# Optimization experiments

Measured on AMD Instinct MI355X. Metric: run time of the kernel, lower is better.

Reference implementation:

```python
import jax, jax.numpy as jnp
import numpy as np

DIM = 512
HEADS = 8
DHEAD = 64
INNER = HEADS * DHEAD
CHUNK = 8
GAMMA = 1.0
EPS = 1e-8
LN_EPS = 1e-5


def setup_inputs() -> dict:
    key = jax.random.key(0)
    ks = jax.random.split(key, 10)
    B, N = 64, 256
    return {
        "q": jax.random.normal(ks[0], (B, N, DIM), jnp.float32),
        "k": jax.random.normal(ks[1], (B, N, DIM), jnp.float32),
        "v": jax.random.normal(ks[2], (B, N, DIM), jnp.float32),
        "ln_gamma": jnp.ones((DIM,), jnp.float32),
        "ln_beta": jnp.zeros((DIM,), jnp.float32),
        "W_in": jax.random.normal(ks[3], (DIM, INNER), jnp.float32) / np.sqrt(DIM),
        "W_out": jax.random.normal(ks[4], (INNER, DIM), jnp.float32) / np.sqrt(INNER),
        "b_out": jnp.zeros((DIM,), jnp.float32),
        "cov_logit": jnp.asarray(0.6, jnp.float32),
        "var_logit": jnp.asarray(0.2, jnp.float32),
        "use_advanced": 1,
    }


def _layernorm(x, g, b):
    mu = jnp.mean(x, axis=-1, keepdims=True)
    var = jnp.mean(jnp.square(x - mu), axis=-1, keepdims=True)
    return (x - mu) * jax.lax.rsqrt(var + LN_EPS) * g + b


def _transform(t, ln_gamma, ln_beta, W_in):
    # [B,N,dim] -> [h,B,N,d]
    B, N, _ = t.shape
    f = _layernorm(t, ln_gamma, ln_beta) @ W_in
    return f.reshape(B, N, HEADS, DHEAD).transpose(2, 0, 1, 3)


def _chunk_stats(E):
    # E: [M, N, d], chunks of size CHUNK over M. Returns per-chunk scalars V, C of shape [M//CHUNK].
    M, N, d = E.shape
    nc = M // CHUNK
    Ec = E.reshape(nc, CHUNK, N, d)
    # variance component: torch.var is unbiased (ddof=1) over seq dim
    sigma = jnp.sqrt(jnp.var(Ec, axis=2, ddof=1) + EPS)  # [nc, CHUNK, d]
    V = jnp.mean(jax.nn.relu(GAMMA - sigma), axis=(1, 2))  # [nc]
    # covariance component: per-sample off-diagonal energy, averaged per chunk
    centered = Ec - jnp.mean(Ec, axis=2, keepdims=True)
    cov = jnp.einsum("csni,csnj->csij", centered, centered) / (N - 1)  # [nc,CHUNK,d,d]
    total = jnp.sum(jnp.square(cov), axis=(2, 3))
    diag = jnp.sum(jnp.square(jnp.diagonal(cov, axis1=2, axis2=3)), axis=2)
    C = jnp.mean((total - diag) / d, axis=1)  # [nc]
    return V, C


def reference(q, k, v, ln_gamma, ln_beta, W_in, W_out, b_out, cov_logit, var_logit, use_advanced):
    f_q = _transform(q, ln_gamma, ln_beta, W_in)  # [h,B,N,d]
    f_k = _transform(k, ln_gamma, ln_beta, W_in)
    f_v = _transform(v, ln_gamma, ln_beta, W_in)
    h, B, N, d = f_q.shape

    # cosine similarity
    dots_qk = jnp.einsum("hbnd,hbmd->hbnm", f_q, f_k)
    qn = jnp.linalg.norm(f_q, axis=-1)  # [h,B,N]
    kn = jnp.linalg.norm(f_k, axis=-1)
    cosine_sim = dots_qk / (qn[..., :, None] * kn[..., None, :])

    if use_advanced:
        Vq, Cq = _chunk_stats(f_q.reshape(h * B, N, d))
        Vk, Ck = _chunk_stats(f_k.reshape(h * B, N, d))
        var_component = jnp.repeat(Vq * Vk, CHUNK).reshape(h, B, 1, 1)
        cov_component = jnp.repeat(Cq * Ck, CHUNK).reshape(h, B, 1, 1)
    else:
        qc = f_q - jnp.mean(f_q, axis=-1, keepdims=True)
        kc = f_k - jnp.mean(f_k, axis=-1, keepdims=True)
        cov_component = jnp.einsum("hbnd,hbmd->hbnm", qc, kc) / d
        q_var = jnp.var(f_q, axis=-1, ddof=1, keepdims=True)  # [h,B,N,1]
        k_var = jnp.var(f_k, axis=-1, ddof=1, keepdims=True)
        var_component = (q_var * jnp.swapaxes(k_var, -1, -2)) / d

    cov_w = jax.nn.sigmoid(cov_logit)
    var_w = jax.nn.sigmoid(var_logit)
    cos_w = 1.0 - cov_w - var_w
    dots = cos_w * cosine_sim + cov_w * cov_component + var_w * var_component
    out = jnp.einsum("hbnm,hbmd->hbnd", dots, f_v)
    out = out.transpose(1, 2, 0, 3).reshape(B, N, h * d)
    return out @ W_out + b_out
```

## Files before the change

### kernel.cpp

```cpp
#include <hip/hip_runtime.h>
#include <cstdint>
#include <cstddef>

#define DIM    512
#define HEADS  8
#define DHEAD  64
#define NSEQ   256
#define BATCH  64
#define NROWS  (BATCH * NSEQ)
#define HB     (HEADS * BATCH)

typedef unsigned short u16;
typedef __bf16 bf16x8 __attribute__((ext_vector_type(8)));
typedef float  f32x4  __attribute__((ext_vector_type(4)));

__device__ __forceinline__ float sigmoidf_(float x) { return 1.0f / (1.0f + expf(-x)); }

__device__ __forceinline__ u16 f2bf(float f) {
    union { float f; unsigned u; } a; a.f = f;
    return (u16)((a.u + 0x7fffu + ((a.u >> 16) & 1u)) >> 16);
}

__device__ __forceinline__ void gload16(const void* g, void* l) {
    __builtin_amdgcn_global_load_lds((const __attribute__((address_space(1))) void*)g,
                                     (__attribute__((address_space(3))) void*)l, 16, 0, 0);
}

__global__ __launch_bounds__(256)
void transpose_cast_kernel(const float* __restrict__ W0, const float* __restrict__ W1,
                           u16* __restrict__ WT)
{
    __shared__ float tile[64][65];
    const int t = threadIdx.x;
    const int bx = blockIdx.x * 64, by = blockIdx.y * 64;
    const float* W = blockIdx.z ? W1 : W0;
    u16* dst = WT + (size_t)blockIdx.z * 512 * 512;
#pragma unroll
    for (int i = 0; i < 16; ++i) {
        int idx = i * 256 + t, r = idx >> 6, c = idx & 63;
        tile[r][c] = W[(size_t)(by + r) * DIM + bx + c];
    }
    __syncthreads();
#pragma unroll
    for (int i = 0; i < 16; ++i) {
        int idx = i * 256 + t, r = idx >> 6, c = idx & 63;
        dst[(size_t)(bx + r) * DIM + by + c] = f2bf(tile[c][r]);
    }
}

__global__ __launch_bounds__(256)
void ln_cast_kernel(const float* __restrict__ qp, const float* __restrict__ kp,
                    const float* __restrict__ vp, const float* __restrict__ gam,
                    const float* __restrict__ bet, u16* __restrict__ out)
{
    const int wid = threadIdx.x >> 6, lane = threadIdx.x & 63;
    const int row = blockIdx.x * 4 + wid;
    const int tns = row >> 14, lr = row & 16383;
    const float* X = (tns == 0) ? qp : (tns == 1) ? kp : vp;
    const float* xr = X + (size_t)lr * DIM;
    float4 a = *(const float4*)(xr + lane * 8);
    float4 b = *(const float4*)(xr + lane * 8 + 4);
    float v[8] = {a.x, a.y, a.z, a.w, b.x, b.y, b.z, b.w};
    float s = 0.f;
#pragma unroll
    for (int i = 0; i < 8; ++i) s += v[i];
#pragma unroll
    for (int o = 32; o > 0; o >>= 1) s += __shfl_xor(s, o, 64);
    const float mu = s * (1.f / DIM);
    float sq = 0.f;
#pragma unroll
    for (int i = 0; i < 8; ++i) { float d = v[i] - mu; sq += d * d; }
#pragma unroll
    for (int o = 32; o > 0; o >>= 1) sq += __shfl_xor(sq, o, 64);
    const float rstd = rsqrtf(sq * (1.f / DIM) + 1e-5f);
    float4 g0 = *(const float4*)(gam + lane * 8), g1 = *(const float4*)(gam + lane * 8 + 4);
    float4 b0 = *(const float4*)(bet + lane * 8), b1 = *(const float4*)(bet + lane * 8 + 4);
    float gv[8] = {g0.x, g0.y, g0.z, g0.w, g1.x, g1.y, g1.z, g1.w};
    float bv[8] = {b0.x, b0.y, b0.z, b0.w, b1.x, b1.y, b1.z, b1.w};
    union { u16 h[8]; uint4 u; } o16;
#pragma unroll
    for (int i = 0; i < 8; ++i) o16.h[i] = f2bf((v[i] - mu) * rstd * gv[i] + bv[i]);
    *(uint4*)(out + (size_t)row * DIM + lane * 8) = o16.u;
}

__global__ __launch_bounds__(256)
void in_gemm_kernel(const u16* __restrict__ A, const u16* __restrict__ BT,
                    u16* __restrict__ FT, u16* __restrict__ Fseq)
{
    __shared__ u16 shm[128 * 136];
    u16* As = shm;
    u16* Bs = shm + 4096;
    u16* Ct = shm;
    const int t = threadIdx.x, lane = t & 63, w = t >> 6;
    const int wr = w >> 1, wc = w & 1;
    const int c0 = blockIdx.x * 128, r0 = blockIdx.y * 128;
    const int cl = lane & 15, q = lane >> 4;

    f32x4 acc[4][4];
#pragma unroll
    for (int i = 0; i < 4; ++i)
#pragma unroll
        for (int j = 0; j < 4; ++j) acc[i][j] = (f32x4){0.f, 0.f, 0.f, 0.f};

    for (int k0 = 0; k0 < DIM; k0 += 32) {
#pragma unroll
        for (int i = 0; i < 2; ++i) {
            int idx = i * 256 + t;
            int row = idx >> 2, ch = idx & 3;
            gload16(A  + (size_t)(r0 + row) * DIM + k0 + ch * 8, As + idx * 8);
            gload16(BT + (size_t)(c0 + row) * DIM + k0 + ch * 8, Bs + idx * 8);
        }
        __syncthreads();
        bf16x8 af[4], bfr[4];
#pragma unroll
        for (int mi = 0; mi < 4; ++mi)
            af[mi] = *(const bf16x8*)(As + (wr * 64 + mi * 16 + cl) * 32 + q * 8);
#pragma unroll
        for (int ni = 0; ni < 4; ++ni)
            bfr[ni] = *(const bf16x8*)(Bs + (wc * 64 + ni * 16 + cl) * 32 + q * 8);
#pragma unroll
        for (int mi = 0; mi < 4; ++mi)
#pragma unroll
            for (int ni = 0; ni < 4; ++ni)
                acc[mi][ni] = __builtin_amdgcn_mfma_f32_16x16x32_bf16(af[mi], bfr[ni],
                                                                      acc[mi][ni], 0, 0, 0);
        __syncthreads();
    }

    const int tns = r0 >> 14, b = (r0 >> 8) & 63, n0 = r0 & 255;
    const int lr0 = r0 & 16383;

    if (tns == 0) {
#pragma unroll
        for (int mi = 0; mi < 4; ++mi) {
            int lrow = wr * 64 + mi * 16 + q * 4;
#pragma unroll
            for (int ni = 0; ni < 4; ++ni) {
                int lcol = wc * 64 + ni * 16 + cl;
#pragma unroll
                for (int r = 0; r < 4; ++r)
                    Ct[(lrow + r) * 136 + lcol] = f2bf(acc[mi][ni][r]);
            }
        }
        __syncthreads();
#pragma unroll
        for (int i = 0; i < 8; ++i) {
            int idx = t + 256 * i, row = idx >> 4, ch = idx & 15;
            *(uint4*)(Fseq + (size_t)(lr0 + row) * DIM + c0 + ch * 8) =
                *(const uint4*)(Ct + row * 136 + ch * 8);
        }
        __syncthreads();
    }
#pragma unroll
    for (int mi = 0; mi < 4; ++mi) {
        int lrow = wr * 64 + mi * 16 + q * 4;
#pragma unroll
        for (int ni = 0; ni < 4; ++ni) {
            int lcol = wc * 64 + ni * 16 + cl;
#pragma unroll
            for (int r = 0; r < 4; ++r)
                Ct[lcol * 136 + lrow + r] = f2bf(acc[mi][ni][r]);
        }
    }
    __syncthreads();
#pragma unroll
    for (int i = 0; i < 8; ++i) {
        int idx = t + 256 * i, lc = idx >> 4, ch = idx & 15;
        *(uint4*)(FT + (((size_t)(tns * 64 + b) * 512 + c0 + lc) * 256 + n0 + ch * 8)) =
            *(const uint4*)(Ct + lc * 136 + ch * 8);
    }
}

__global__ __launch_bounds__(256)
void stats_kernel(const u16* __restrict__ FT, float* __restrict__ norms,
                  float2* __restrict__ vc)
{
    __shared__ u16 ET[64 * 264];
    __shared__ float mu[64];
    __shared__ float red[4][64];
    __shared__ float wr3[4][3];
    const int hb = blockIdx.x, tns = blockIdx.y, h = hb >> 6, b = hb & 63;
    const int t = threadIdx.x, lane = t & 63, w = t >> 6, cl = lane & 15, q = lane >> 4;
    const size_t Fb = ((size_t)(tns * 64 + b) * 512 + h * 64) * 256;

#pragma unroll
    for (int i = 0; i < 8; ++i) {
        int idx = t + 256 * i;
        int row = idx >> 5, ch = idx & 31;
        *(bf16x8*)(ET + row * 264 + ch * 8) =
            *(const bf16x8*)(FT + Fb + (size_t)row * 256 + ch * 8);
    }
    __syncthreads();

    {
        float s = 0.f;
#pragma unroll
        for (int d = 0; d < 64; ++d) {
            float x = (float)*(const __bf16*)(ET + d * 264 + t);
            s += x * x;
        }
        norms[((size_t)tns * HB + hb) * 256 + t] = sqrtf(s);
    }
    {
        int d = t & 63, part = t >> 6;
        float s = 0.f;
#pragma unroll
        for (int i = 0; i < 8; ++i) {
            bf16x8 v8 = *(const bf16x8*)(ET + d * 264 + part * 64 + i * 8);
#pragma unroll
            for (int j = 0; j < 8; ++j) s += (float)v8[j];
        }
        red[part][d] = s;
    }
    __syncthreads();
    if (t < 64) mu[t] = (red[0][t] + red[1][t] + red[2][t] + red[3][t]) * (1.f / 256.f);
    __syncthreads();

    f32x4 g[4];
#pragma unroll
    for (int nj = 0; nj < 4; ++nj) g[nj] = (f32x4){0.f, 0.f, 0.f, 0.f};
#pragma unroll
    for (int ks = 0; ks < 8; ++ks) {
        bf16x8 af = *(const bf16x8*)(ET + (16 * w + cl) * 264 + ks * 32 + q * 8);
#pragma unroll
        for (int nj = 0; nj < 4; ++nj) {
            bf16x8 bfr = *(const bf16x8*)(ET + (16 * nj + cl) * 264 + ks * 32 + q * 8);
            g[nj] = __builtin_amdgcn_mfma_f32_16x16x32_bf16(af, bfr, g[nj], 0, 0, 0);
        }
    }
    float t2 = 0.f, d2 = 0.f, vs = 0.f;
#pragma unroll
    for (int nj = 0; nj < 4; ++nj) {
        int j = 16 * nj + cl;
        float mj = mu[j];
#pragma unroll
        for (int r = 0; r < 4; ++r) {
            int i = 16 * w + 4 * q + r;
            float gc = (g[nj][r] - 256.f * mu[i] * mj) * (1.f / 255.f);
            float g2 = gc * gc;
            t2 += g2;
            if (i == j) {
                d2 += g2;
                float sig = sqrtf(gc + 1e-8f);
                vs += fmaxf(1.f - sig, 0.f);
            }
        }
    }
#pragma unroll
    for (int o = 32; o > 0; o >>= 1) {
        t2 += __shfl_xor(t2, o, 64);
        d2 += __shfl_xor(d2, o, 64);
        vs += __shfl_xor(vs, o, 64);
    }
    if (lane == 0) { wr3[w][0] = t2; wr3[w][1] = d2; wr3[w][2] = vs; }
    __syncthreads();
    if (t == 0) {
        float T = 0.f, D = 0.f, V = 0.f;
        for (int i = 0; i < 4; ++i) { T += wr3[i][0]; D += wr3[i][1]; V += wr3[i][2]; }
        vc[(size_t)tns * HB + hb] = make_float2(V * (1.f / 64.f), (T - D) * (1.f / 64.f));
    }
}

__global__ __launch_bounds__(256)
void attn_kernel(const u16* __restrict__ FT, const u16* __restrict__ Fseq,
                 const float* __restrict__ norms, const float2* __restrict__ vc,
                 const float* __restrict__ cov_logit, const float* __restrict__ var_logit,
                 u16* __restrict__ G)
{
    __shared__ u16 pool[256 * 72];
    __shared__ u16 MT[64 * 72];
    __shared__ float invq[256], invk[256], sv[64];
    const int hb = blockIdx.x, h = hb >> 6, b = hb & 63;
    const int t = threadIdx.x, lane = t & 63, w = t >> 6, cl = lane & 15, q = lane >> 4;
    u16* KT = pool;
    u16* VT = pool + 64 * 136;

    const float cw = sigmoidf_(*cov_logit), vw = sigmoidf_(*var_logit);
    const float cosw = 1.f - cw - vw;
    float s_hb;
    {
        int basec = hb & ~7;
        float vq = 0, cq = 0, vk = 0, ck = 0;
#pragma unroll
        for (int m = 0; m < 8; ++m) {
            float2 a = vc[basec + m];       vq += a.x; cq += a.y;
            float2 bb = vc[HB + basec + m]; vk += bb.x; ck += bb.y;
        }
        s_hb = (cw * cq * ck + vw * vq * vk) * (1.f / 64.f);
    }

    invq[t] = 1.f / norms[((size_t)0 * HB + hb) * 256 + t];
    invk[t] = 1.f / norms[((size_t)1 * HB + hb) * 256 + t];
    __syncthreads();

    const size_t FTk = ((size_t)(1 * 64 + b) * 512 + h * 64) * 256;
    const size_t FTv = ((size_t)(2 * 64 + b) * 512 + h * 64) * 256;
    f32x4 acc1[4];
#pragma unroll
    for (int nj = 0; nj < 4; ++nj) acc1[nj] = (f32x4){0.f, 0.f, 0.f, 0.f};
    float sp[4] = {0.f, 0.f, 0.f, 0.f};

    for (int c = 0; c < 2; ++c) {
#pragma unroll
        for (int i = 0; i < 4; ++i) {
            int idx = t + 256 * i;
            int row = idx >> 4, ch = idx & 15;
            int n0 = c * 128 + ch * 8;
            bf16x8 kv = *(const bf16x8*)(FT + FTk + (size_t)row * 256 + n0);
            bf16x8 vv = *(const bf16x8*)(FT + FTv + (size_t)row * 256 + n0);
            bf16x8 ksc;
#pragma unroll
            for (int j = 0; j < 8; ++j) ksc[j] = (__bf16)((float)kv[j] * invk[n0 + j]);
            *(bf16x8*)(KT + row * 136 + ch * 8) = ksc;
            *(bf16x8*)(VT + row * 136 + ch * 8) = vv;
        }
        __syncthreads();
#pragma unroll
        for (int ks = 0; ks < 4; ++ks) {
            bf16x8 af = *(const bf16x8*)(KT + (16 * w + cl) * 136 + ks * 32 + q * 8);
#pragma unroll
            for (int nj = 0; nj < 4; ++nj) {
                bf16x8 bfr = *(const bf16x8*)(VT + (16 * nj + cl) * 136 + ks * 32 + q * 8);
                if (w == 0) {
                    float s = 0.f;
#pragma unroll
                    for (int j = 0; j < 8; ++j) s += (float)bfr[j];
                    sp[nj] += s;
                }
                acc1[nj] = __builtin_amdgcn_mfma_f32_16x16x32_bf16(af, bfr, acc1[nj], 0, 0, 0);
            }
        }
        __syncthreads();
    }
    if (w == 0) {
#pragma unroll
        for (int nj = 0; nj < 4; ++nj) {
            float s = sp[nj];
            s += __shfl_xor(s, 16, 64);
            s += __shfl_xor(s, 32, 64);
            if (q == 0) sv[16 * nj + cl] = s;
        }
    }
#pragma unroll
    for (int nj = 0; nj < 4; ++nj)
#pragma unroll
        for (int r = 0; r < 4; ++r)
            MT[(16 * nj + cl) * 72 + 16 * w + 4 * q + r] = f2bf(acc1[nj][r]);
    __syncthreads();

    f32x4 acc2[4][4];
#pragma unroll
    for (int mi = 0; mi < 4; ++mi)
#pragma unroll
        for (int nj = 0; nj < 4; ++nj) acc2[mi][nj] = (f32x4){0.f, 0.f, 0.f, 0.f};
    const size_t Fq = (size_t)(b * 256) * DIM + h * 64;
#pragma unroll
    for (int ks2 = 0; ks2 < 2; ++ks2) {
        bf16x8 bfm[4];
#pragma unroll
        for (int nj = 0; nj < 4; ++nj)
            bfm[nj] = *(const bf16x8*)(MT + (16 * nj + cl) * 72 + ks2 * 32 + q * 8);
#pragma unroll
        for (int mi = 0; mi < 4; ++mi) {
            bf16x8 aq = *(const bf16x8*)(Fseq + Fq +
                         (size_t)(64 * w + 16 * mi + cl) * DIM + ks2 * 32 + q * 8);
#pragma unroll
            for (int nj = 0; nj < 4; ++nj)
                acc2[mi][nj] = __builtin_amdgcn_mfma_f32_16x16x32_bf16(aq, bfm[nj],
                                                                       acc2[mi][nj], 0, 0, 0);
        }
    }
    __syncthreads();
    u16* Os = pool;
#pragma unroll
    for (int mi = 0; mi < 4; ++mi) {
        int nbase = 64 * w + 16 * mi + 4 * q;
#pragma unroll
        for (int nj = 0; nj < 4; ++nj) {
            int j = 16 * nj + cl;
            float svj = sv[j];
#pragma unroll
            for (int r = 0; r < 4; ++r) {
                float o = cosw * acc2[mi][nj][r] * invq[nbase + r] + s_hb * svj;
                Os[(nbase + r) * 72 + j] = f2bf(o);
            }
        }
    }
    __syncthreads();
#pragma unroll
    for (int i = 0; i < 8; ++i) {
        int cidx = t + 256 * i;
        int row = cidx >> 3, ch = cidx & 7;
        *(uint4*)(G + (size_t)(b * 256 + row) * DIM + h * 64 + ch * 8) =
            *(const uint4*)(Os + row * 72 + ch * 8);
    }
}

__global__ __launch_bounds__(256)
void out_gemm_kernel(const u16* __restrict__ A, const u16* __restrict__ BT,
                     const float* __restrict__ bias, float* __restrict__ C)
{
    __shared__ u16 As[128 * 32];
    __shared__ u16 Bs[128 * 32];
    const int t = threadIdx.x, lane = t & 63, w = t >> 6;
    const int wr = w >> 1, wc = w & 1;
    const int c0 = blockIdx.x * 128, r0 = blockIdx.y * 128;
    const int cl = lane & 15, q = lane >> 4;

    f32x4 acc[4][4];
#pragma unroll
    for (int i = 0; i < 4; ++i)
#pragma unroll
        for (int j = 0; j < 4; ++j) acc[i][j] = (f32x4){0.f, 0.f, 0.f, 0.f};

    for (int k0 = 0; k0 < DIM; k0 += 32) {
#pragma unroll
        for (int i = 0; i < 2; ++i) {
            int idx = i * 256 + t;
            int row = idx >> 2, ch = idx & 3;
            gload16(A  + (size_t)(r0 + row) * DIM + k0 + ch * 8, As + idx * 8);
            gload16(BT + (size_t)(c0 + row) * DIM + k0 + ch * 8, Bs + idx * 8);
        }
        __syncthreads();
        bf16x8 af[4], bfr[4];
#pragma unroll
        for (int mi = 0; mi < 4; ++mi)
            af[mi] = *(const bf16x8*)(As + (wr * 64 + mi * 16 + cl) * 32 + q * 8);
#pragma unroll
        for (int ni = 0; ni < 4; ++ni)
            bfr[ni] = *(const bf16x8*)(Bs + (wc * 64 + ni * 16 + cl) * 32 + q * 8);
#pragma unroll
        for (int mi = 0; mi < 4; ++mi)
#pragma unroll
            for (int ni = 0; ni < 4; ++ni)
                acc[mi][ni] = __builtin_amdgcn_mfma_f32_16x16x32_bf16(af[mi], bfr[ni],
                                                                      acc[mi][ni], 0, 0, 0);
        __syncthreads();
    }
#pragma unroll
    for (int mi = 0; mi < 4; ++mi) {
        int row0 = r0 + wr * 64 + mi * 16 + q * 4;
#pragma unroll
        for (int ni = 0; ni < 4; ++ni) {
            int col = c0 + wc * 64 + ni * 16 + cl;
            float bv = bias[col];
#pragma unroll
            for (int r = 0; r < 4; ++r)
                C[(size_t)(row0 + r) * DIM + col] = acc[mi][ni][r] + bv;
        }
    }
}

extern "C" void kernel_launch(void* const* d_in, const int* in_sizes, int n_in,
                              void* d_out, int out_size, void* d_ws, size_t ws_size,
                              hipStream_t stream)
{
    const float* q         = (const float*)d_in[0];
    const float* k         = (const float*)d_in[1];
    const float* v         = (const float*)d_in[2];
    const float* ln_g      = (const float*)d_in[3];
    const float* ln_b      = (const float*)d_in[4];
    const float* W_in      = (const float*)d_in[5];
    const float* W_out     = (const float*)d_in[6];
    const float* b_out     = (const float*)d_in[7];
    const float* cov_logit = (const float*)d_in[8];
    const float* var_logit = (const float*)d_in[9];
    float* out = (float*)d_out;

    char* base = (char*)d_ws;
    u16*    Abf   = (u16*)base;
    u16*    WT    = (u16*)(base + 50331648);
    u16*    FT    = (u16*)(base + 51380224);
    u16*    Fseq  = (u16*)(base + 101711872);
    float*  norms = (float*)(base + 118489088);
    float2* vc    = (float2*)(base + 119537664);
    u16*    Gb    = Abf;

    transpose_cast_kernel<<<dim3(8, 8, 2), 256, 0, stream>>>(W_in, W_out, WT);
    ln_cast_kernel<<<dim3(3 * NROWS / 4), 256, 0, stream>>>(q, k, v, ln_g, ln_b, Abf);
    in_gemm_kernel<<<dim3(4, 3 * NROWS / 128), 256, 0, stream>>>(Abf, WT, FT, Fseq);
    stats_kernel<<<dim3(HB, 2), 256, 0, stream>>>(FT, norms, vc);
    attn_kernel<<<dim3(HB), 256, 0, stream>>>(FT, Fseq, norms, vc,
                                              cov_logit, var_logit, Gb);
    out_gemm_kernel<<<dim3(4, NROWS / 128), 256, 0, stream>>>(
        Gb, WT + 512 * 512, b_out, out);
}
```

Baseline: 245.1 us.

## Fold LayerNorm into input GEMM via weight prescaling and epilogue correction

```diff
diff --git a/kernel.cpp b/kernel.cpp
--- a/kernel.cpp
+++ b/kernel.cpp
@@ -28,13 +28,16 @@
 
 __global__ __launch_bounds__(256)
 void transpose_cast_kernel(const float* __restrict__ W0, const float* __restrict__ W1,
-                           u16* __restrict__ WT)
+                           const float* __restrict__ gam, const float* __restrict__ bet,
+                           u16* __restrict__ WT, float* __restrict__ cs,
+                           float* __restrict__ bW)
 {
     __shared__ float tile[64][65];
     const int t = threadIdx.x;
     const int bx = blockIdx.x * 64, by = blockIdx.y * 64;
-    const float* W = blockIdx.z ? W1 : W0;
-    u16* dst = WT + (size_t)blockIdx.z * 512 * 512;
+    const int z = blockIdx.z;
+    const float* W = z ? W1 : W0;
+    u16* dst = WT + (size_t)z * 512 * 512;
 #pragma unroll
     for (int i = 0; i < 16; ++i) {
         int idx = i * 256 + t, r = idx >> 6, c = idx & 63;
@@ -44,77 +47,83 @@
 #pragma unroll
     for (int i = 0; i < 16; ++i) {
         int idx = i * 256 + t, r = idx >> 6, c = idx & 63;
-        dst[(size_t)(bx + r) * DIM + by + c] = f2bf(tile[c][r]);
+        float wv = tile[c][r];
+        if (!z) wv *= gam[by + c];
+        dst[(size_t)(bx + r) * DIM + by + c] = f2bf(wv);
+    }
+    if (!z && t < 64) {
+        float s1 = 0.f, s2 = 0.f;
+#pragma unroll 8
+        for (int r = 0; r < 64; ++r) {
+            float wv = tile[r][t];
+            s1 += gam[by + r] * wv;
+            s2 += bet[by + r] * wv;
+        }
+        atomicAdd(cs + bx + t, s1);
+        atomicAdd(bW + bx + t, s2);
     }
 }
 
 __global__ __launch_bounds__(256)
-void ln_cast_kernel(const float* __restrict__ qp, const float* __restrict__ kp,
-                    const float* __restrict__ vp, const float* __restrict__ gam,
-                    const float* __restrict__ bet, u16* __restrict__ out)
-{
-    const int wid = threadIdx.x >> 6, lane = threadIdx.x & 63;
-    const int row = blockIdx.x * 4 + wid;
-    const int tns = row >> 14, lr = row & 16383;
-    const float* X = (tns == 0) ? qp : (tns == 1) ? kp : vp;
-    const float* xr = X + (size_t)lr * DIM;
-    float4 a = *(const float4*)(xr + lane * 8);
-    float4 b = *(const float4*)(xr + lane * 8 + 4);
-    float v[8] = {a.x, a.y, a.z, a.w, b.x, b.y, b.z, b.w};
-    float s = 0.f;
-#pragma unroll
-    for (int i = 0; i < 8; ++i) s += v[i];
-#pragma unroll
-    for (int o = 32; o > 0; o >>= 1) s += __shfl_xor(s, o, 64);
-    const float mu = s * (1.f / DIM);
-    float sq = 0.f;
-#pragma unroll
-    for (int i = 0; i < 8; ++i) { float d = v[i] - mu; sq += d * d; }
-#pragma unroll
-    for (int o = 32; o > 0; o >>= 1) sq += __shfl_xor(sq, o, 64);
-    const float rstd = rsqrtf(sq * (1.f / DIM) + 1e-5f);
-    float4 g0 = *(const float4*)(gam + lane * 8), g1 = *(const float4*)(gam + lane * 8 + 4);
-    float4 b0 = *(const float4*)(bet + lane * 8), b1 = *(const float4*)(bet + lane * 8 + 4);
-    float gv[8] = {g0.x, g0.y, g0.z, g0.w, g1.x, g1.y, g1.z, g1.w};
-    float bv[8] = {b0.x, b0.y, b0.z, b0.w, b1.x, b1.y, b1.z, b1.w};
-    union { u16 h[8]; uint4 u; } o16;
-#pragma unroll
-    for (int i = 0; i < 8; ++i) o16.h[i] = f2bf((v[i] - mu) * rstd * gv[i] + bv[i]);
-    *(uint4*)(out + (size_t)row * DIM + lane * 8) = o16.u;
-}
-
-__global__ __launch_bounds__(256)
-void in_gemm_kernel(const u16* __restrict__ A, const u16* __restrict__ BT,
+void in_gemm_kernel(const float* __restrict__ Xq, const float* __restrict__ Xk,
+                    const float* __restrict__ Xv, const u16* __restrict__ BT,
+                    const float* __restrict__ cs, const float* __restrict__ bW,
                     u16* __restrict__ FT, u16* __restrict__ Fseq)
 {
-    __shared__ u16 shm[128 * 136];
-    u16* As = shm;
-    u16* Bs = shm + 4096;
-    u16* Ct = shm;
+    __shared__ __align__(16) u16 shm[128 * 136];
+    __shared__ float muL[128], rsL[128];
+    float* Asf = (float*)shm;
+    u16*  Bs   = shm + 8192;
+    u16*  Ct   = shm;
     const int t = threadIdx.x, lane = t & 63, w = t >> 6;
     const int wr = w >> 1, wc = w & 1;
-    const int c0 = blockIdx.x * 128, r0 = blockIdx.y * 128;
+    const int flat = blockIdx.y * 4 + blockIdx.x;
+    const int rt = (flat & 7) * 48 + ((flat >> 3) >> 2);
+    const int c0 = ((flat >> 3) & 3) * 128;
+    const int r0 = rt * 128;
     const int cl = lane & 15, q = lane >> 4;
+    const int tns = r0 >> 14, lr0 = r0 & 16383;
+    const float* X = (tns == 0) ? Xq : (tns == 1) ? Xk : Xv;
 
     f32x4 acc[4][4];
 #pragma unroll
     for (int i = 0; i < 4; ++i)
 #pragma unroll
         for (int j = 0; j < 4; ++j) acc[i][j] = (f32x4){0.f, 0.f, 0.f, 0.f};
+    float s1[4] = {0.f, 0.f, 0.f, 0.f}, s2[4] = {0.f, 0.f, 0.f, 0.f};
 
     for (int k0 = 0; k0 < DIM; k0 += 32) {
+#pragma unroll
+        for (int i = 0; i < 4; ++i) {
+            int idx = i * 256 + t;
+            int row = idx >> 3, chs = idx & 7;
+            int chg = chs ^ (row & 7);
+            gload16(X + (size_t)(lr0 + row) * DIM + k0 + chg * 4, (char*)shm + idx * 16);
+        }
 #pragma unroll
         for (int i = 0; i < 2; ++i) {
             int idx = i * 256 + t;
             int row = idx >> 2, ch = idx & 3;
-            gload16(A  + (size_t)(r0 + row) * DIM + k0 + ch * 8, As + idx * 8);
             gload16(BT + (size_t)(c0 + row) * DIM + k0 + ch * 8, Bs + idx * 8);
         }
         __syncthreads();
         bf16x8 af[4], bfr[4];
 #pragma unroll
-        for (int mi = 0; mi < 4; ++mi)
-            af[mi] = *(const bf16x8*)(As + (wr * 64 + mi * 16 + cl) * 32 + q * 8);
+        for (int mi = 0; mi < 4; ++mi) {
+            int rl = wr * 64 + mi * 16 + cl;
+            int slo = (2 * q) ^ (rl & 7);
+            float4 fl = ((const float4*)Asf)[rl * 8 + slo];
+            float4 fh = ((const float4*)Asf)[rl * 8 + (slo ^ 1)];
+            if (wc == 0) {
+                s1[mi] += (fl.x + fl.y) + (fl.z + fl.w) + (fh.x + fh.y) + (fh.z + fh.w);
+                s2[mi] += fl.x * fl.x + fl.y * fl.y + fl.z * fl.z + fl.w * fl.w
+                        + fh.x * fh.x + fh.y * fh.y + fh.z * fh.z + fh.w * fh.w;
+            }
+            af[mi][0] = (__bf16)fl.x; af[mi][1] = (__bf16)fl.y;
+            af[mi][2] = (__bf16)fl.z; af[mi][3] = (__bf16)fl.w;
+            af[mi][4] = (__bf16)fh.x; af[mi][5] = (__bf16)fh.y;
+            af[mi][6] = (__bf16)fh.z; af[mi][7] = (__bf16)fh.w;
+        }
 #pragma unroll
         for (int ni = 0; ni < 4; ++ni)
             bfr[ni] = *(const bf16x8*)(Bs + (wc * 64 + ni * 16 + cl) * 32 + q * 8);
@@ -127,8 +136,43 @@
         __syncthreads();
     }
 
-    const int tns = r0 >> 14, b = (r0 >> 8) & 63, n0 = r0 & 255;
-    const int lr0 = r0 & 16383;
+    if (wc == 0) {
+#pragma unroll
+        for (int mi = 0; mi < 4; ++mi) {
+            float a = s1[mi], b = s2[mi];
+            a += __shfl_xor(a, 16, 64); a += __shfl_xor(a, 32, 64);
+            b += __shfl_xor(b, 16, 64); b += __shfl_xor(b, 32, 64);
+            if (q == 0) {
+                int rl = wr * 64 + mi * 16 + cl;
+                float mu = a * (1.f / DIM);
+                float var = b * (1.f / DIM) - mu * mu;
+                muL[rl] = mu;
+                rsL[rl] = rsqrtf(var + 1e-5f);
+            }
+        }
+    }
+    __syncthreads();
+
+    {
+        float csv[4], bwv[4];
+#pragma unroll
+        for (int ni = 0; ni < 4; ++ni) {
+            int col = c0 + wc * 64 + ni * 16 + cl;
+            csv[ni] = cs[col]; bwv[ni] = bW[col];
+        }
+#pragma unroll
+        for (int mi = 0; mi < 4; ++mi)
+#pragma unroll
+            for (int r = 0; r < 4; ++r) {
+                int rl = wr * 64 + mi * 16 + q * 4 + r;
+                float mu = muL[rl], rs = rsL[rl];
+#pragma unroll
+                for (int ni = 0; ni < 4; ++ni)
+                    acc[mi][ni][r] = rs * (acc[mi][ni][r] - mu * csv[ni]) + bwv[ni];
+            }
+    }
+
+    const int b = (r0 >> 8) & 63, n0 = r0 & 255;
 
     if (tns == 0) {
 #pragma unroll
@@ -404,7 +448,10 @@
     __shared__ u16 Bs[128 * 32];
     const int t = threadIdx.x, lane = t & 63, w = t >> 6;
     const int wr = w >> 1, wc = w & 1;
-    const int c0 = blockIdx.x * 128, r0 = blockIdx.y * 128;
+    const int flat = blockIdx.y * 4 + blockIdx.x;
+    const int rt = (flat & 7) * 16 + ((flat >> 3) >> 2);
+    const int c0 = ((flat >> 3) & 3) * 128;
+    const int r0 = rt * 128;
     const int cl = lane & 15, q = lane >> 4;
 
     f32x4 acc[4][4];
@@ -468,17 +515,20 @@
     float* out = (float*)d_out;
 
     char* base = (char*)d_ws;
-    u16*    Abf   = (u16*)base;
-    u16*    WT    = (u16*)(base + 50331648);
-    u16*    FT    = (u16*)(base + 51380224);
-    u16*    Fseq  = (u16*)(base + 101711872);
-    float*  norms = (float*)(base + 118489088);
-    float2* vc    = (float2*)(base + 119537664);
-    u16*    Gb    = Abf;
-
-    transpose_cast_kernel<<<dim3(8, 8, 2), 256, 0, stream>>>(W_in, W_out, WT);
-    ln_cast_kernel<<<dim3(3 * NROWS / 4), 256, 0, stream>>>(q, k, v, ln_g, ln_b, Abf);
-    in_gemm_kernel<<<dim3(4, 3 * NROWS / 128), 256, 0, stream>>>(Abf, WT, FT, Fseq);
+    u16*    FT    = (u16*)base;
+    u16*    Fseq  = (u16*)(base + 50331648);
+    u16*    Gb    = (u16*)(base + 67108864);
+    u16*    WT    = (u16*)(base + 83886080);
+    float*  norms = (float*)(base + 84934656);
+    float2* vc    = (float2*)(base + 85983232);
+    float*  cs    = (float*)(base + 85991424);
+    float*  bW    = cs + 512;
+
+    hipMemsetAsync(cs, 0, 4096, stream);
+    transpose_cast_kernel<<<dim3(8, 8, 2), 256, 0, stream>>>(W_in, W_out, ln_g, ln_b,
+                                                             WT, cs, bW);
+    in_gemm_kernel<<<dim3(4, 3 * NROWS / 128), 256, 0, stream>>>(q, k, v, WT, cs, bW,
+                                                                 FT, Fseq);
     stats_kernel<<<dim3(HB, 2), 256, 0, stream>>>(FT, norms, vc);
     attn_kernel<<<dim3(HB), 256, 0, stream>>>(FT, Fseq, norms, vc,
                                               cov_logit, var_logit, Gb);
```

Result: slower. 259.3 us (+5.8%).
